# Kernel tuning notes

Hardware: AMD Instinct MI355X
Metric: run time of the kernel (lower is better)

Reference implementation:

```python
import jax, jax.numpy as jnp
import numpy as np

LN_EPS = 1e-5


def setup_inputs() -> dict:
    key = jax.random.key(0)
    k_h, k_e, k_w, k_b = jax.random.split(key, 4)
    N, E, D_IN, D_OUT = 10000, 640000, 128, 128
    H = jax.random.normal(k_h, (N, D_IN), dtype=jnp.float32)
    edge_index = jax.random.randint(k_e, (2, E), 0, N, dtype=jnp.int64)
    # Linear params (torch default init: U(-1/sqrt(fan_in), 1/sqrt(fan_in)))
    bound = 1.0 / np.sqrt(D_IN)
    W = jax.random.uniform(k_w, (D_OUT, D_IN), minval=-bound, maxval=bound, dtype=jnp.float32)
    b = jax.random.uniform(k_b, (D_OUT,), minval=-bound, maxval=bound, dtype=jnp.float32)
    gamma = jnp.ones((D_OUT,), dtype=jnp.float32)
    beta = jnp.zeros((D_OUT,), dtype=jnp.float32)
    return {"H": H, "edge_index": edge_index, "num_nodes": N,
            "W": W, "b": b, "gamma": gamma, "beta": beta}


def reference(H, edge_index, num_nodes, W, b, gamma, beta):
    # Append self-loops
    self_loops = jnp.arange(num_nodes, dtype=edge_index.dtype)
    row = jnp.concatenate([edge_index[0], self_loops])  # sources (gather)
    col = jnp.concatenate([edge_index[1], self_loops])  # destinations (scatter)

    # Degree over row indices (matches torch scatter_add_ on row)
    deg = jax.ops.segment_sum(jnp.ones_like(row, dtype=H.dtype), row,
                              num_segments=num_nodes)
    deg_inv = 1.0 / jnp.maximum(deg, 1.0)

    # gather-scale-scatter_add aggregation: H_agg[col] += H[row] * deg_inv[row]
    msgs = H[row] * deg_inv[row][:, None]  # (E+N, D_in)
    H_agg = jax.ops.segment_sum(msgs, col, num_segments=num_nodes)

    # Linear + ReLU (dropout is identity in eval)
    H_out = jax.nn.relu(H_agg @ W.T + b)

    # LayerNorm over features
    mu = jnp.mean(H_out, axis=-1, keepdims=True)
    var = jnp.var(H_out, axis=-1, keepdims=True)
    return (H_out - mu) * jax.lax.rsqrt(var + LN_EPS) * gamma + beta
```

## Files before the change

### kernel.cpp

```cpp
#include <hip/hip_runtime.h>


#define DFEAT 128
#define MAXN 10240
#define NBLK 128
#define PAD 160
#define SPLIT 8
#define KPT (NBLK / SPLIT)

__device__ __forceinline__ unsigned bf16rne(float f) {
    unsigned u = __float_as_uint(f);
    return (u + 0x7fffu + ((u >> 16) & 1u)) >> 16;
}
__device__ __forceinline__ float bflo(unsigned u) { return __uint_as_float(u << 16); }
__device__ __forceinline__ float bfhi(unsigned u) { return __uint_as_float(u & 0xffff0000u); }

__global__ __launch_bounds__(1024) void hist_pack_kernel(
    const int* __restrict__ ei, int E, int Epb, int N,
    const float* __restrict__ W, int* __restrict__ packedHist,
    unsigned short* __restrict__ rank16, unsigned* __restrict__ WbT) {
    __shared__ unsigned h[MAXN];
    int t = threadIdx.x, b = blockIdx.x;
    for (int i = t; i < N; i += 1024) h[i] = 0u;
    __syncthreads();
    {
        int e0 = b * Epb, e1 = min(E, e0 + Epb);
        for (int e = e0 + t; e < e1; e += 1024) {
            atomicAdd(&h[ei[e]], 1u);
            unsigned old = atomicAdd(&h[ei[E + e]], 0x10000u);
            rank16[e] = (unsigned short)(old >> 16);
        }
    }
    __syncthreads();
    for (int i = t; i < N; i += 1024) packedHist[b * N + i] = (int)h[i];
    {
        int gid = b * 1024 + t;
        if (gid < 128 * (DFEAT / 2)) {
            int k2 = gid >> 7, d = gid & 127;
            WbT[gid] = bf16rne(W[d * 128 + 2 * k2]) |
                       (bf16rne(W[d * 128 + 2 * k2 + 1]) << 16);
        }
    }
}

__global__ __launch_bounds__(256) void colscan_kernel(
    int* __restrict__ packedHist, float* __restrict__ dinv,
    int* __restrict__ cnt, int N) {
    int tid = blockIdx.x * 256 + threadIdx.x;
    int b = tid >> 3, p = tid & 7;
    if (b >= N) return;
    int lane = threadIdx.x & 63;
    int base = p * KPT;
    int sR = 0, sC = 0;
#pragma unroll
    for (int j = 0; j < KPT; ++j) {
        unsigned v = (unsigned)packedHist[(base + j) * N + b];
        sR += (int)(v & 0xffffu);
        sC += (int)(v >> 16);
    }
    int incl = sC;
    int u1 = __shfl_up(incl, 1); if (p >= 1) incl += u1;
    int u2 = __shfl_up(incl, 2); if (p >= 2) incl += u2;
    int u4 = __shfl_up(incl, 4); if (p >= 4) incl += u4;
    int gExcl = incl - sC;
    int totC = __shfl(incl, lane | 7);
    int tR = sR;
    tR += __shfl_xor(tR, 1);
    tR += __shfl_xor(tR, 2);
    tR += __shfl_xor(tR, 4);
    int run = gExcl;
#pragma unroll
    for (int j = 0; j < KPT; ++j) {
        unsigned v = (unsigned)packedHist[(base + j) * N + b];
        packedHist[(base + j) * N + b] = run;
        run += (int)(v >> 16);
    }
    if (p == 0) {
        dinv[b] = 1.0f / (float)(tR + 1);
        cnt[b] = min(totC, PAD);
    }
}

__global__ __launch_bounds__(256) void fillscale_kernel(
    const int* __restrict__ ei, int E, int Epb, int N,
    const int* __restrict__ blkpref, const unsigned short* __restrict__ rank16,
    unsigned short* __restrict__ edge_src,
    const float* __restrict__ H, const float* __restrict__ dinv,
    unsigned* __restrict__ HsU, int subPerBlk) {
    {
        int tid = blockIdx.x * 256 + threadIdx.x;
        int total = N * (DFEAT / 2);
        int stride = gridDim.x * 256;
        const float2* __restrict__ H2 = (const float2*)H;
        for (int i = tid; i < total; i += stride) {
            float d = dinv[i >> 6];
            float2 hh = H2[i];
            HsU[i] = bf16rne(hh.x * d) | (bf16rne(hh.y * d) << 16);
        }
    }
    int b = blockIdx.x / subPerBlk;
    int sub = blockIdx.x - b * subPerBlk;
    if (b < NBLK) {
        int e0 = b * Epb, e1 = min(E, e0 + Epb);
        const int* __restrict__ pre = blkpref + b * N;
        int stride = subPerBlk * 256;
        for (int e = e0 + sub * 256 + threadIdx.x; e < e1; e += stride) {
            int c = ei[E + e];
            int slot = pre[c] + (int)rank16[e];
            if (slot < PAD)
                edge_src[c * PAD + slot] = (unsigned short)ei[e];
        }
    }
}

__global__ __launch_bounds__(256) void aggmmln_kernel(
    const unsigned* __restrict__ HsU, const unsigned* __restrict__ WbT,
    const int* __restrict__ cnt, const unsigned short* __restrict__ edge_src,
    const float* __restrict__ bias, const float* __restrict__ gamma,
    const float* __restrict__ beta, float* __restrict__ out, int N) {
    __shared__ float rows[4][DFEAT];
    int t = threadIdx.x;
    int w = t >> 6, l = t & 63;
    int c = blockIdx.x * 4 + w;

    float x = 0.f, y = 0.f;
    if (c < N) {
        unsigned su = HsU[c * 64 + l];
        x = bflo(su);
        y = bfhi(su);
        int deg = cnt[c];
        const unsigned short* __restrict__ es = edge_src + c * PAD;
        int e = 0;
        for (; e + 8 <= deg; e += 8) {
            uint4 iv = *(const uint4*)(es + e);
            int s0 = iv.x & 0xffff, s1 = iv.x >> 16;
            int s2 = iv.y & 0xffff, s3 = iv.y >> 16;
            int s4 = iv.z & 0xffff, s5 = iv.z >> 16;
            int s6 = iv.w & 0xffff, s7 = iv.w >> 16;
            unsigned u0 = HsU[s0 * 64 + l], u1 = HsU[s1 * 64 + l];
            unsigned u2 = HsU[s2 * 64 + l], u3 = HsU[s3 * 64 + l];
            unsigned u4 = HsU[s4 * 64 + l], u5 = HsU[s5 * 64 + l];
            unsigned u6 = HsU[s6 * 64 + l], u7 = HsU[s7 * 64 + l];
            x += bflo(u0) + bflo(u1) + bflo(u2) + bflo(u3) +
                 bflo(u4) + bflo(u5) + bflo(u6) + bflo(u7);
            y += bfhi(u0) + bfhi(u1) + bfhi(u2) + bfhi(u3) +
                 bfhi(u4) + bfhi(u5) + bfhi(u6) + bfhi(u7);
        }
        for (; e < deg; ++e) {
            unsigned u = HsU[(int)es[e] * 64 + l];
            x += bflo(u);
            y += bfhi(u);
        }
    }
    *(float2*)&rows[w][2 * l] = make_float2(x, y);
    asm volatile("s_waitcnt lgkmcnt(0)" ::: "memory");
    __builtin_amdgcn_sched_barrier(0);

    float a0 = bias[l], a1 = bias[l + 64];
#pragma unroll 8
    for (int k2 = 0; k2 < 64; ++k2) {
        unsigned wA = WbT[k2 * 128 + l];
        unsigned wB = WbT[k2 * 128 + l + 64];
        float2 xv = *(const float2*)&rows[w][2 * k2];
        a0 += xv.x * bflo(wA) + xv.y * bfhi(wA);
        a1 += xv.x * bflo(wB) + xv.y * bfhi(wB);
    }
    float v0 = fmaxf(a0, 0.f), v1 = fmaxf(a1, 0.f);
    float s = v0 + v1, q = v0 * v0 + v1 * v1;
    for (int o = 32; o; o >>= 1) {
        s += __shfl_xor(s, o);
        q += __shfl_xor(q, o);
    }
    float mean = s * (1.0f / 128.0f);
    float var = q * (1.0f / 128.0f) - mean * mean;
    float rstd = rsqrtf(var + 1e-5f);
    if (c < N) {
        out[(size_t)c * 128 + l] = (v0 - mean) * rstd * gamma[l] + beta[l];
        out[(size_t)c * 128 + l + 64] =
            (v1 - mean) * rstd * gamma[l + 64] + beta[l + 64];
    }
}

extern "C" void kernel_launch(void* const* d_in, const int* in_sizes, int n_in,
                              void* d_out, int out_size, void* d_ws, size_t ws_size,
                              hipStream_t stream) {
    const float* H = (const float*)d_in[0];
    const int* ei = (const int*)d_in[1];
    const float* W = (const float*)d_in[3];
    const float* bias = (const float*)d_in[4];
    const float* gamma = (const float*)d_in[5];
    const float* beta = (const float*)d_in[6];
    float* out = (float*)d_out;

    const int N = in_sizes[0] / DFEAT;
    const int E = in_sizes[1] / 2;
    const int Epb = (E + NBLK - 1) / NBLK;

    char* wp = (char*)d_ws;
    auto alloc = [&](size_t bytes) {
        char* p = wp;
        wp += (bytes + 255) & ~(size_t)255;
        return p;
    };
    int* packedHist = (int*)alloc((size_t)NBLK * N * 4);
    unsigned short* rank16 = (unsigned short*)alloc((size_t)E * 2);
    unsigned short* edge_src = (unsigned short*)alloc((size_t)N * PAD * 2);
    unsigned* HsU = (unsigned*)alloc((size_t)N * (DFEAT / 2) * 4);
    unsigned* WbT = (unsigned*)alloc((size_t)128 * (DFEAT / 2) * 4);
    int* cnt = (int*)alloc((size_t)N * 4);
    float* dinv = (float*)alloc((size_t)N * 4);
    (void)ws_size;

    hist_pack_kernel<<<NBLK, 1024, 0, stream>>>(ei, E, Epb, N, W,
                                                packedHist, rank16, WbT);
    colscan_kernel<<<(N * SPLIT + 255) / 256, 256, 0, stream>>>(
        packedHist, dinv, cnt, N);
    {
        int subPerBlk = 8;
        fillscale_kernel<<<NBLK * subPerBlk, 256, 0, stream>>>(
            ei, E, Epb, N, packedHist, rank16, edge_src, H, dinv, HsU, subPerBlk);
    }
    aggmmln_kernel<<<(N + 3) / 4, 256, 0, stream>>>(
        HsU, WbT, cnt, edge_src, bias, gamma, beta, out, N);
}
```

Measured before the change: 64.14 us.

## Fuse H scaling into colscan and broadcast aggregated row via readlane

Moves the bf16 scaling of H by inverse degree into the column-scan kernel, so each node's row is scaled right where its degree is computed. This drops the dinv buffer and its reload in the fill kernel. In the aggregation kernel, the LDS staging of the aggregated row is replaced by readlane broadcasts inside the matmul loop, and that loop's unroll goes from 8 to 16. This removes the LDS round trip and wait, at the cost of scalar readlane instructions that may serialize on the scalar unit.

```diff
diff --git a/kernel.cpp b/kernel.cpp
--- a/kernel.cpp
+++ b/kernel.cpp
@@ -44,8 +44,8 @@
 }
 
 __global__ __launch_bounds__(256) void colscan_kernel(
-    int* __restrict__ packedHist, float* __restrict__ dinv,
-    int* __restrict__ cnt, int N) {
+    int* __restrict__ packedHist, const float* __restrict__ H,
+    unsigned* __restrict__ HsU, int* __restrict__ cnt, int N) {
     int tid = blockIdx.x * 256 + threadIdx.x;
     int b = tid >> 3, p = tid & 7;
     if (b >= N) return;
@@ -75,41 +75,34 @@
         packedHist[(base + j) * N + b] = run;
         run += (int)(v >> 16);
     }
-    if (p == 0) {
-        dinv[b] = 1.0f / (float)(tR + 1);
-        cnt[b] = min(totC, PAD);
-    }
-}
-
-__global__ __launch_bounds__(256) void fillscale_kernel(
+    {
+        float d = 1.0f / (float)(tR + 1);
+        const float2* __restrict__ H2 = (const float2*)H;
+#pragma unroll
+        for (int j = 0; j < 8; ++j) {
+            int idx = b * 64 + j * 8 + p;
+            float2 hh = H2[idx];
+            HsU[idx] = bf16rne(hh.x * d) | (bf16rne(hh.y * d) << 16);
+        }
+    }
+    if (p == 0) cnt[b] = min(totC, PAD);
+}
+
+__global__ __launch_bounds__(256) void fill_kernel(
     const int* __restrict__ ei, int E, int Epb, int N,
     const int* __restrict__ blkpref, const unsigned short* __restrict__ rank16,
-    unsigned short* __restrict__ edge_src,
-    const float* __restrict__ H, const float* __restrict__ dinv,
-    unsigned* __restrict__ HsU, int subPerBlk) {
-    {
-        int tid = blockIdx.x * 256 + threadIdx.x;
-        int total = N * (DFEAT / 2);
-        int stride = gridDim.x * 256;
-        const float2* __restrict__ H2 = (const float2*)H;
-        for (int i = tid; i < total; i += stride) {
-            float d = dinv[i >> 6];
-            float2 hh = H2[i];
-            HsU[i] = bf16rne(hh.x * d) | (bf16rne(hh.y * d) << 16);
-        }
-    }
+    unsigned short* __restrict__ edge_src, int subPerBlk) {
     int b = blockIdx.x / subPerBlk;
     int sub = blockIdx.x - b * subPerBlk;
-    if (b < NBLK) {
-        int e0 = b * Epb, e1 = min(E, e0 + Epb);
-        const int* __restrict__ pre = blkpref + b * N;
-        int stride = subPerBlk * 256;
-        for (int e = e0 + sub * 256 + threadIdx.x; e < e1; e += stride) {
-            int c = ei[E + e];
-            int slot = pre[c] + (int)rank16[e];
-            if (slot < PAD)
-                edge_src[c * PAD + slot] = (unsigned short)ei[e];
-        }
+    if (b >= NBLK) return;
+    int e0 = b * Epb, e1 = min(E, e0 + Epb);
+    const int* __restrict__ pre = blkpref + b * N;
+    int stride = subPerBlk * 256;
+    for (int e = e0 + sub * 256 + threadIdx.x; e < e1; e += stride) {
+        int c = ei[E + e];
+        int slot = pre[c] + (int)rank16[e];
+        if (slot < PAD)
+            edge_src[c * PAD + slot] = (unsigned short)ei[e];
     }
 }
 
@@ -118,18 +111,17 @@
     const int* __restrict__ cnt, const unsigned short* __restrict__ edge_src,
     const float* __restrict__ bias, const float* __restrict__ gamma,
     const float* __restrict__ beta, float* __restrict__ out, int N) {
-    __shared__ float rows[4][DFEAT];
     int t = threadIdx.x;
     int w = t >> 6, l = t & 63;
     int c = blockIdx.x * 4 + w;
-
-    float x = 0.f, y = 0.f;
-    if (c < N) {
-        unsigned su = HsU[c * 64 + l];
-        x = bflo(su);
-        y = bfhi(su);
-        int deg = cnt[c];
-        const unsigned short* __restrict__ es = edge_src + c * PAD;
+    bool live = c < N;
+    int cc = live ? c : 0;
+
+    unsigned su = HsU[cc * 64 + l];
+    float x = bflo(su), y = bfhi(su);
+    {
+        int deg = live ? cnt[cc] : 0;
+        const unsigned short* __restrict__ es = edge_src + cc * PAD;
         int e = 0;
         for (; e + 8 <= deg; e += 8) {
             uint4 iv = *(const uint4*)(es + e);
@@ -152,18 +144,16 @@
             y += bfhi(u);
         }
     }
-    *(float2*)&rows[w][2 * l] = make_float2(x, y);
-    asm volatile("s_waitcnt lgkmcnt(0)" ::: "memory");
-    __builtin_amdgcn_sched_barrier(0);
 
     float a0 = bias[l], a1 = bias[l + 64];
-#pragma unroll 8
+#pragma unroll 16
     for (int k2 = 0; k2 < 64; ++k2) {
+        float sx = __uint_as_float(__builtin_amdgcn_readlane(__float_as_uint(x), k2));
+        float sy = __uint_as_float(__builtin_amdgcn_readlane(__float_as_uint(y), k2));
         unsigned wA = WbT[k2 * 128 + l];
         unsigned wB = WbT[k2 * 128 + l + 64];
-        float2 xv = *(const float2*)&rows[w][2 * k2];
-        a0 += xv.x * bflo(wA) + xv.y * bfhi(wA);
-        a1 += xv.x * bflo(wB) + xv.y * bfhi(wB);
+        a0 += sx * bflo(wA) + sy * bfhi(wA);
+        a1 += sx * bflo(wB) + sy * bfhi(wB);
     }
     float v0 = fmaxf(a0, 0.f), v1 = fmaxf(a1, 0.f);
     float s = v0 + v1, q = v0 * v0 + v1 * v1;
@@ -174,7 +164,7 @@
     float mean = s * (1.0f / 128.0f);
     float var = q * (1.0f / 128.0f) - mean * mean;
     float rstd = rsqrtf(var + 1e-5f);
-    if (c < N) {
+    if (live) {
         out[(size_t)c * 128 + l] = (v0 - mean) * rstd * gamma[l] + beta[l];
         out[(size_t)c * 128 + l + 64] =
             (v1 - mean) * rstd * gamma[l + 64] + beta[l + 64];
@@ -208,17 +198,16 @@
     unsigned* HsU = (unsigned*)alloc((size_t)N * (DFEAT / 2) * 4);
     unsigned* WbT = (unsigned*)alloc((size_t)128 * (DFEAT / 2) * 4);
     int* cnt = (int*)alloc((size_t)N * 4);
-    float* dinv = (float*)alloc((size_t)N * 4);
     (void)ws_size;
 
     hist_pack_kernel<<<NBLK, 1024, 0, stream>>>(ei, E, Epb, N, W,
                                                 packedHist, rank16, WbT);
     colscan_kernel<<<(N * SPLIT + 255) / 256, 256, 0, stream>>>(
-        packedHist, dinv, cnt, N);
+        packedHist, H, HsU, cnt, N);
     {
         int subPerBlk = 8;
-        fillscale_kernel<<<NBLK * subPerBlk, 256, 0, stream>>>(
-            ei, E, Epb, N, packedHist, rank16, edge_src, H, dinv, HsU, subPerBlk);
+        fill_kernel<<<NBLK * subPerBlk, 256, 0, stream>>>(
+            ei, E, Epb, N, packedHist, rank16, edge_src, subPerBlk);
     }
     aggmmln_kernel<<<(N + 3) / 4, 256, 0, stream>>>(
         HsU, WbT, cnt, edge_src, bias, gamma, beta, out, N);
```

After: 68.30 us. +6.5%, slower.
